# Kernel tuning notes

Measured on AMD Instinct MI355X. Metric: run time of the kernel, lower is better.

Reference implementation:

```python
import math
import jax, jax.numpy as jnp
import numpy as np

BIG_K = 13
SMALL_K = 5
C_OUT = 256
C_IN = 768
NK = math.ceil(BIG_K / SMALL_K)  # 3
PAD = (SMALL_K - 1) - SMALL_K // 2  # extra_pad = padding - small_kernel//2 = 2


def _make_one_hot_kernel(group_idx: int) -> np.ndarray:
    """Replicates PureAddShiftMP._make_one_hot_kernels: (C_OUT, C_IN, NK, NK)."""
    nk = NK
    kH = kW = nk
    weight = np.zeros((C_OUT, C_IN, kH, kW), dtype=np.float32)
    sq = int(math.ceil(math.sqrt(nk)))
    base_positions = [(k // sq, k % sq) for k in range(nk)]
    for i in range(C_OUT):
        for k in range(nk):
            in_idx = (i * nk + k) % C_IN
            perm_k = (k + group_idx) % nk
            row, col = base_positions[perm_k]
            weight[i, in_idx, row % kH, col % kW] = 1.0
    return weight

K0 = jnp.asarray(_make_one_hot_kernel(0))
K1 = jnp.asarray(_make_one_hot_kernel(1))
K2 = jnp.asarray(_make_one_hot_kernel(2))


def _conv(x, w):
    # NCHW x OIHW -> NCHW, stride 1, symmetric padding PAD
    return jax.lax.conv_general_dilated(
        x, w, window_strides=(1, 1), padding=[(PAD, PAD), (PAD, PAD)],
        dimension_numbers=("NCHW", "OIHW", "NCHW"))


def _crop_to(out, H, W):
    Ht, Wt = out.shape[2], out.shape[3]
    if Ht > H or Wt > W:
        sh = (Ht - H) // 2
        sw = (Wt - W) // 2
        out = out[:, :, sh:sh + H, sw:sw + W]
    if out.shape[2] != H or out.shape[3] != W:
        out = jax.image.resize(out, (out.shape[0], out.shape[1], H, W), method="nearest")
    return out


def setup_inputs() -> dict:
    key = jax.random.key(0)
    x = jax.random.normal(key, (8, C_IN, 64, 64), dtype=jnp.float32)
    return {"x": x, "b": 8, "hout": 64, "wout": 64}


def reference(x, b, hout, wout):
    out0 = _crop_to(_conv(x, K0), hout, wout)
    out1 = _crop_to(_conv(x, K1), hout, wout)
    out2 = _crop_to(_conv(x, K2), hout, wout)
    return (out0, out1, out2)
```

## Files before the change

kernel.cpp:

```cpp
#include <hip/hip_runtime.h>


#define CIN 768
#define COUT 256
#define PER_GROUP 8388608L

typedef float f4 __attribute__((ext_vector_type(4)));

__global__ __launch_bounds__(256) void shift3_kernel(
    const float* __restrict__ xin, float* __restrict__ out)
{
    unsigned t = blockIdx.x * 256u + threadIdx.x;
    int xq = (int)(t & 15);
    int yy = (int)((t >> 4) & 63);
    int o  = (int)((t >> 10) & 255);
    int n  = (int)(t >> 18);
    int x0 = xq << 2;

    const float* base = xin + (((size_t)n * CIN + 3 * (size_t)o) << 12);
    const float ymask = (yy == 0) ? 0.0f : 1.0f;
    const float xmask = (xq == 0) ? 0.0f : 1.0f;
    const int rm = ((yy == 0) ? 0 : (yy - 1)) << 6;
    const int r  = yy << 6;

    f4 p0[3], p1[3], p2[3];
    #pragma unroll
    for (int k = 0; k < 3; ++k) {
        const float* c = base + (k << 12);
        f4 M = *reinterpret_cast<const f4*>(c + rm + x0);
        f4 R = *reinterpret_cast<const f4*>(c + r + x0);
        M.x *= ymask; M.y *= ymask; M.z *= ymask; M.w *= ymask;
        float m0 = __shfl_up(M.w, 1, 64) * xmask;
        float r0 = __shfl_up(R.w, 1, 64) * xmask;
        p1[k] = M;
        p0[k] = (f4){m0, M.x, M.y, M.z};
        p2[k] = (f4){r0, R.x, R.y, R.z};
    }

    f4 o0 = p0[0] + p1[1] + p2[2];
    f4 o1 = p1[0] + p2[1] + p0[2];
    f4 o2 = p2[0] + p0[1] + p1[2];

    size_t oidx = (((size_t)n * COUT + (size_t)o) << 12) + ((size_t)yy << 6) + (size_t)x0;
    __builtin_nontemporal_store(o0, reinterpret_cast<f4*>(out + oidx));
    __builtin_nontemporal_store(o1, reinterpret_cast<f4*>(out + oidx + PER_GROUP));
    __builtin_nontemporal_store(o2, reinterpret_cast<f4*>(out + oidx + 2 * PER_GROUP));
}

extern "C" void kernel_launch(void* const* d_in, const int* in_sizes, int n_in,
                              void* d_out, int out_size, void* d_ws, size_t ws_size,
                              hipStream_t stream) {
    const float* x = (const float*)d_in[0];
    float* out = (float*)d_out;
    shift3_kernel<<<8192, 256, 0, stream>>>(x, out);
}
```

Before: 34.34 us.

## Process four rows per thread, reusing previous row in registers

New measurement: 37.40 us. 1.09x slower.

```diff
diff --git a/kernel.cpp b/kernel.cpp
--- a/kernel.cpp
+++ b/kernel.cpp
@@ -1,8 +1,6 @@
 #include <hip/hip_runtime.h>
 
 
-#define CIN 768
-#define COUT 256
 #define PER_GROUP 8388608L
 
 typedef float f4 __attribute__((ext_vector_type(4)));
@@ -12,39 +10,53 @@
 {
     unsigned t = blockIdx.x * 256u + threadIdx.x;
     int xq = (int)(t & 15);
-    int yy = (int)((t >> 4) & 63);
-    int o  = (int)((t >> 10) & 255);
-    int n  = (int)(t >> 18);
+    int s  = (int)((t >> 4) & 15);
+    int o  = (int)((t >> 8) & 255);
+    int n  = (int)(t >> 16);
     int x0 = xq << 2;
+    int y0 = s << 2;
 
-    const float* base = xin + (((size_t)n * CIN + 3 * (size_t)o) << 12);
-    const float ymask = (yy == 0) ? 0.0f : 1.0f;
+    const float* base = xin + (((size_t)n * 768 + 3 * (size_t)o) << 12);
+    const float ymask = (s == 0) ? 0.0f : 1.0f;
     const float xmask = (xq == 0) ? 0.0f : 1.0f;
-    const int rm = ((yy == 0) ? 0 : (yy - 1)) << 6;
-    const int r  = yy << 6;
+    const int rowm = ((s == 0) ? 0 : (y0 - 1)) << 6;
 
-    f4 p0[3], p1[3], p2[3];
-    #pragma unroll
-    for (int k = 0; k < 3; ++k) {
-        const float* c = base + (k << 12);
-        f4 M = *reinterpret_cast<const f4*>(c + rm + x0);
-        f4 R = *reinterpret_cast<const f4*>(c + r + x0);
-        M.x *= ymask; M.y *= ymask; M.z *= ymask; M.w *= ymask;
-        float m0 = __shfl_up(M.w, 1, 64) * xmask;
-        float r0 = __shfl_up(R.w, 1, 64) * xmask;
-        p1[k] = M;
-        p0[k] = (f4){m0, M.x, M.y, M.z};
-        p2[k] = (f4){r0, R.x, R.y, R.z};
+    f4 A0, A1, A2; float a0s, a1s, a2s;
+    {
+        const float* r = base + rowm + x0;
+        A0 = *reinterpret_cast<const f4*>(r);
+        A1 = *reinterpret_cast<const f4*>(r + 4096);
+        A2 = *reinterpret_cast<const f4*>(r + 8192);
+        A0 *= ymask; A1 *= ymask; A2 *= ymask;
+        a0s = __shfl_up(A0.w, 1, 64) * xmask;
+        a1s = __shfl_up(A1.w, 1, 64) * xmask;
+        a2s = __shfl_up(A2.w, 1, 64) * xmask;
     }
 
-    f4 o0 = p0[0] + p1[1] + p2[2];
-    f4 o1 = p1[0] + p2[1] + p0[2];
-    f4 o2 = p2[0] + p0[1] + p1[2];
+    size_t obase = (((size_t)n * 256 + (size_t)o) << 12) + ((size_t)y0 << 6) + (size_t)x0;
 
-    size_t oidx = (((size_t)n * COUT + (size_t)o) << 12) + ((size_t)yy << 6) + (size_t)x0;
-    __builtin_nontemporal_store(o0, reinterpret_cast<f4*>(out + oidx));
-    __builtin_nontemporal_store(o1, reinterpret_cast<f4*>(out + oidx + PER_GROUP));
-    __builtin_nontemporal_store(o2, reinterpret_cast<f4*>(out + oidx + 2 * PER_GROUP));
+    #pragma unroll
+    for (int j = 0; j < 4; ++j) {
+        const float* r = base + ((y0 + j) << 6) + x0;
+        f4 B0 = *reinterpret_cast<const f4*>(r);
+        f4 B1 = *reinterpret_cast<const f4*>(r + 4096);
+        f4 B2 = *reinterpret_cast<const f4*>(r + 8192);
+        float b0s = __shfl_up(B0.w, 1, 64) * xmask;
+        float b1s = __shfl_up(B1.w, 1, 64) * xmask;
+        float b2s = __shfl_up(B2.w, 1, 64) * xmask;
+
+        f4 o0 = (f4){a0s, A0.x, A0.y, A0.z} + A1 + (f4){b2s, B2.x, B2.y, B2.z};
+        f4 o1 = A0 + (f4){b1s, B1.x, B1.y, B1.z} + (f4){a2s, A2.x, A2.y, A2.z};
+        f4 o2 = (f4){b0s, B0.x, B0.y, B0.z} + (f4){a1s, A1.x, A1.y, A1.z} + A2;
+
+        float* op = out + obase + ((size_t)j << 6);
+        __builtin_nontemporal_store(o0, reinterpret_cast<f4*>(op));
+        __builtin_nontemporal_store(o1, reinterpret_cast<f4*>(op + PER_GROUP));
+        __builtin_nontemporal_store(o2, reinterpret_cast<f4*>(op + 2 * PER_GROUP));
+
+        A0 = B0; A1 = B1; A2 = B2;
+        a0s = b0s; a1s = b1s; a2s = b2s;
+    }
 }
 
 extern "C" void kernel_launch(void* const* d_in, const int* in_sizes, int n_in,
@@ -52,5 +64,5 @@
                               hipStream_t stream) {
     const float* x = (const float*)d_in[0];
     float* out = (float*)d_out;
-    shift3_kernel<<<8192, 256, 0, stream>>>(x, out);
+    shift3_kernel<<<2048, 256, 0, stream>>>(x, out);
 }
```
